# Optimization experiments

Measured on AMD Instinct MI355X. Metric: run time of the kernel, lower is better.

## Reference

```python
import jax, jax.numpy as jnp
import numpy as np

# --- fake-quant helpers (Brevitas-style simulated int4 with STE) ---

def _fq(x, scale, qmin, qmax):
    # fake quantize with straight-through estimator
    q = jnp.clip(jnp.round(x / scale), qmin, qmax) * scale
    return x + jax.lax.stop_gradient(q - x)

def quant_act_signed4(x):
    # signed 4-bit symmetric activation quant: scale = max|x| / 7
    scale = jax.lax.stop_gradient(jnp.maximum(jnp.max(jnp.abs(x)), 1e-8) / 7.0)
    return _fq(x, scale, -8, 7), scale

def quant_relu4(x):
    # QuantReLU: relu then unsigned 4-bit quant, scale = max / 15
    x = jax.nn.relu(x)
    scale = jax.lax.stop_gradient(jnp.maximum(jnp.max(x), 1e-8) / 15.0)
    return _fq(x, scale, 0, 15), scale

def quant_w4(w):
    # per-tensor symmetric 4-bit weight quant
    scale = jax.lax.stop_gradient(jnp.maximum(jnp.max(jnp.abs(w)), 1e-8) / 7.0)
    return _fq(w, scale, -8, 7), scale

def quant_bias32(b, in_scale, w_scale):
    # Int32Bias: bias quantized at scale = input_scale * weight_scale
    s = in_scale * w_scale
    return _fq(b, s, -(2.0**31), 2.0**31 - 1.0)

def conv2d(x, w, b):
    y = jax.lax.conv_general_dilated(x, w, (1, 1), 'VALID',
                                     dimension_numbers=('NCHW', 'OIHW', 'NCHW'))
    return y + b[None, :, None, None]


def setup_inputs() -> dict:
    key = jax.random.key(0)
    ks = jax.random.split(key, 9)
    f32 = jnp.float32
    return {
        'x':   jax.random.normal(ks[0], (32, 3, 224, 224), f32),
        'w1':  jax.random.normal(ks[1], (32, 3, 3, 3), f32) * 0.1,
        'b1':  jax.random.normal(ks[2], (32,), f32) * 0.05,
        'w2':  jax.random.normal(ks[3], (64, 32, 3, 3), f32) * 0.06,
        'b2':  jax.random.normal(ks[4], (64,), f32) * 0.05,
        'wf1': jax.random.normal(ks[5], (128, 64), f32) * 0.1,
        'bf1': jax.random.normal(ks[6], (128,), f32) * 0.05,
        'wf2': jax.random.normal(ks[7], (10, 128), f32) * 0.08,
        'bf2': jax.random.normal(ks[8], (10,), f32) * 0.05,
    }


def reference(x, w1, b1, w2, b2, wf1, bf1, wf2, bf2):
    # quant_inp
    xq, s_in = quant_act_signed4(x)
    # conv1 (quantized weights, Int32 bias)
    w1q, sw1 = quant_w4(w1)
    y = conv2d(xq, w1q, quant_bias32(b1, s_in, sw1))
    y, s1 = quant_relu4(y)
    # conv2
    w2q, sw2 = quant_w4(w2)
    y = conv2d(y, w2q, quant_bias32(b2, s1, sw2))
    y, s2 = quant_relu4(y)
    # adaptive avg pool to 1x1 + flatten -> [B, 64]
    y = jnp.mean(y, axis=(2, 3))
    # fc1
    wf1q, swf1 = quant_w4(wf1)
    y = y @ wf1q.T + quant_bias32(bf1, s2, swf1)
    y, s3 = quant_relu4(y)
    # fc2
    wf2q, swf2 = quant_w4(wf2)
    y = y @ wf2q.T + quant_bias32(bf2, s3, swf2)
    return jax.nn.log_softmax(y, axis=1)
```

## Files before the change

kernel.cpp:

```cpp
#include <hip/hip_runtime.h>
#include <cstdint>
#include <cstddef>

#define DI __device__ __forceinline__

typedef int v4i  __attribute__((ext_vector_type(4)));
typedef int v16i __attribute__((ext_vector_type(16)));

#if defined(__has_builtin)
#if __has_builtin(__builtin_amdgcn_sdot4)
#define HAS_SDOT4 1
#endif
#if __has_builtin(__builtin_amdgcn_alignbyte)
#define HAS_ALIGNBYTE 1
#endif
#if __has_builtin(__builtin_amdgcn_global_load_lds)
#define HAS_GLLDS 1
#endif
#if __has_builtin(__builtin_amdgcn_perm)
#define HAS_PERM 1
#endif
#endif

DI int dot4(unsigned a, unsigned b, int c) {
#ifdef HAS_SDOT4
  return __builtin_amdgcn_sdot4((int)a, (int)b, c, false);
#else
#pragma unroll
  for (int k = 0; k < 4; ++k)
    c += (int)(signed char)(a >> (8 * k)) * (int)(signed char)(b >> (8 * k));
  return c;
#endif
}

DI unsigned alignb(unsigned hi, unsigned lo, int sh) {
#ifdef HAS_ALIGNBYTE
  return __builtin_amdgcn_alignbyte(hi, lo, sh);
#else
  return sh ? ((lo >> (8 * sh)) | (hi << (32 - 8 * sh))) : lo;
#endif
}

DI unsigned bperm(unsigned hi, unsigned lo, unsigned sel) {
#ifdef HAS_PERM
  return __builtin_amdgcn_perm(hi, lo, sel);
#else
  unsigned r = 0;
#pragma unroll
  for (int i = 0; i < 4; ++i) {
    unsigned s = (sel >> (8 * i)) & 255u;
    unsigned b = (s < 4) ? (lo >> (8 * s)) : (hi >> (8 * (s - 4)));
    r |= (b & 255u) << (8 * i);
  }
  return r;
#endif
}

DI float qclamp(int a, float h) {
  return fminf(fmaxf(rintf((float)a * h), 0.f), 15.f);
}

DI unsigned pack4(float4 v, float s) {
  float f[4] = {v.x, v.y, v.z, v.w};
  unsigned w = 0;
#pragma unroll
  for (int k = 0; k < 4; ++k) {
    float q = rintf(f[k] / s);
    q = fminf(fmaxf(q, -8.f), 7.f);
    w |= ((unsigned)((int)q & 255)) << (8 * k);
  }
  return w;
}

#ifdef HAS_GLLDS
typedef __attribute__((address_space(1))) void glb_void;
typedef __attribute__((address_space(3))) void lds_void;
DI void gl_lds16(const void* g, void* l) {
  __builtin_amdgcn_global_load_lds((const glb_void*)g, (lds_void*)l, 16, 0, 0);
}
#else
DI void gl_lds16(const void* g, void* l) { *(v4i*)l = *(const v4i*)g; }
#endif

struct Scal {
  unsigned max_x, max_w1, max_w2, max_wf1, max_wf2;
  int max1, max2;
};

DI float mkscale(unsigned bits, float d) { return fmaxf(__uint_as_float(bits), 1e-8f) / d; }
DI float d_s_in(const Scal* sc) { return mkscale(sc->max_x, 7.f); }
DI float d_sw1(const Scal* sc)  { return mkscale(sc->max_w1, 7.f); }
DI float d_sw2(const Scal* sc)  { return mkscale(sc->max_w2, 7.f); }
DI float d_s1(const Scal* sc)   { return fmaxf((float)sc->max1 * (d_s_in(sc) * d_sw1(sc)), 1e-8f) / 15.f; }
DI float d_s2(const Scal* sc)   { return fmaxf((float)sc->max2 * (d_s1(sc) * d_sw2(sc)), 1e-8f) / 15.f; }

static constexpr int NX   = 32 * 3 * 224 * 224;
static constexpr int NP1  = 32 * 32 * 222 * 224;
static constexpr int C2_ROWB   = 224 * 32;
static constexpr int C2_HPLANE = 224 * 16;
static constexpr int C2V_BLK   = 1120;
static constexpr int C2V_ROWS  = 22;

DI float wave_maxf(float v) { for (int o = 32; o; o >>= 1) v = fmaxf(v, __shfl_down(v, o, 64)); return v; }
DI int   wave_maxi(int v)   { for (int o = 32; o; o >>= 1) v = max(v, __shfl_down(v, o, 64));   return v; }

DI float block_maxf(float v) {
  __shared__ float s[8];
  v = wave_maxf(v);
  int lane = threadIdx.x & 63, w = threadIdx.x >> 6;
  int nw = (int)(blockDim.x >> 6);
  if (!lane) s[w] = v;
  __syncthreads();
  if (threadIdx.x < 64) {
    float t = ((int)threadIdx.x < nw) ? s[threadIdx.x] : 0.f;
    v = wave_maxf(t);
  }
  return v;
}

DI int block_maxi(int v) {
  __shared__ int s[8];
  v = wave_maxi(v);
  int lane = threadIdx.x & 63, w = threadIdx.x >> 6;
  int nw = (int)(blockDim.x >> 6);
  if (!lane) s[w] = v;
  __syncthreads();
  if (threadIdx.x < 64) {
    int t = ((int)threadIdx.x < nw) ? s[threadIdx.x] : 0;
    v = wave_maxi(t);
  }
  return v;
}

__global__ void k_absmax_xw(const float4* __restrict__ x, int n4,
                            const float* __restrict__ w1, const float* __restrict__ w2,
                            const float* __restrict__ wf1, const float* __restrict__ wf2,
                            Scal* sc) {
  if (blockIdx.x < 1024) {
    float m = 0.f;
    for (int i = blockIdx.x * 256 + threadIdx.x; i < n4; i += 1024 * 256) {
      float4 v = x[i];
      m = fmaxf(m, fmaxf(fmaxf(fabsf(v.x), fabsf(v.y)), fmaxf(fabsf(v.z), fabsf(v.w))));
    }
    m = block_maxf(m);
    if (!threadIdx.x) atomicMax(&sc->max_x, __float_as_uint(m));
    return;
  }
  const float* p; int n; unsigned* slot;
  int wb = blockIdx.x - 1024;
  if (wb == 0)      { p = w1;  n = 864;   slot = &sc->max_w1; }
  else if (wb == 1) { p = w2;  n = 18432; slot = &sc->max_w2; }
  else if (wb == 2) { p = wf1; n = 8192;  slot = &sc->max_wf1; }
  else              { p = wf2; n = 1280;  slot = &sc->max_wf2; }
  float m = 0.f;
  for (int i = threadIdx.x; i < n; i += 256) m = fmaxf(m, fabsf(p[i]));
  m = block_maxf(m);
  if (!threadIdx.x) atomicMax(slot, __float_as_uint(m));
}


DI void kpack0(const unsigned* R, v4i& f) {
  f[0] = (int)bperm(R[1], R[0], 0x04020100u);
  f[1] = (int)bperm(R[2], R[1], 0x05040201u);
  f[2] = (int)bperm(R[3], R[2], 0x06050402u);
  f[3] = (int)bperm(R[5], R[4], 0x04020100u);
}
DI void kpack1(const unsigned* R, v4i& f) {
  f[0] = (int)bperm(R[1], R[0], 0x05040201u);
  f[1] = (int)bperm(R[2], R[1], 0x06050402u);
  f[2] = (int)bperm(0u,   R[3], 0x04020100u);
  f[3] = 0;
}

DI v4i conv1_afrag(const unsigned* lw, int oc, int lhalf) {
  unsigned R[6];
  v4i f;
  if (lhalf == 0) {
#pragma unroll
    for (int s = 0; s < 6; ++s) R[s] = lw[oc * 9 + s];
    kpack0(R, f);
  } else {
#pragma unroll
    for (int s = 0; s < 4; ++s) R[s] = lw[oc * 9 + 5 + s];
    kpack1(R, f);
  }
  return f;
}

DI v4i conv1_bfrag(const signed char* lx, int oh_l, int qb, int sh, int lhalf) {
  unsigned R[6];
  v4i f;
  if (lhalf == 0) {
#pragma unroll
    for (int s = 0; s < 6; ++s) {
      int ic = s / 3, kh = s - ic * 3;
      const signed char* base = lx + (ic * 8 + oh_l + kh) * 224 + qb;
      unsigned d0 = *(const unsigned*)base;
      unsigned d1 = *(const unsigned*)(base + 4);
      R[s] = alignb(d1, d0, sh);
    }
    kpack0(R, f);
  } else {
#pragma unroll
    for (int s = 0; s < 4; ++s) {
      int seg = 5 + s;
      int ic = seg / 3, kh = seg - ic * 3;
      const signed char* base = lx + (ic * 8 + oh_l + kh) * 224 + qb;
      unsigned d0 = *(const unsigned*)base;
      unsigned d1 = *(const unsigned*)(base + 4);
      R[s] = alignb(d1, d0, sh);
    }
    kpack1(R, f);
  }
  return f;
}

DI void conv1_stage(const float4* x, const float* w1, const float* b1,
                    int b, int oh0, int tid, float s_in, float sw1,
                    signed char* lx, unsigned* lw, int* lb) {
  for (int i = tid; i < 288; i += 448) {
    int oc = i / 9, r = i - oc * 9;
    unsigned w = 0;
#pragma unroll
    for (int k = 0; k < 3; ++k) {
      float q = rintf(w1[oc * 27 + r * 3 + k] / sw1);
      q = fminf(fmaxf(q, -8.f), 7.f);
      w |= ((unsigned)((int)q & 255)) << (8 * k);
    }
    lw[i] = w;
  }
  if (tid < 32) lb[tid] = (int)rintf(b1[tid] / (s_in * sw1));
  const float4* src = x + (size_t)b * 3 * 224 * 56;
  unsigned* dst = (unsigned*)lx;
#pragma unroll
  for (int it = 0; it < 3; ++it) {
    int i = it * 448 + tid;
    int row = i / 56, d = i - row * 56;
    int ic = row >> 3, r = row & 7;
    dst[i] = pack4(src[(ic * 224 + (oh0 + r)) * 56 + d], s_in);
  }
}

__global__ void __launch_bounds__(448) k_conv1a(
    const float4* __restrict__ x, const float* __restrict__ w1,
    const float* __restrict__ b1, const float* __restrict__ w2,
    const Scal* __restrict__ sc, unsigned* __restrict__ w2frag,
    int* __restrict__ max1) {
  int tid = threadIdx.x;
  if (blockIdx.x >= 1184) {
    int j = (blockIdx.x - 1184) * 448 + tid;
    if (j < 4608) {
      int icq = j & 7; int t = j >> 3;
      int kw = t % 3; t /= 3;
      int kh = t % 3; int oc = t / 3;
      float s = d_sw2(sc);
      unsigned w = 0;
#pragma unroll
      for (int k = 0; k < 4; ++k) {
        int ic = icq * 4 + k;
        float q = rintf(w2[(oc * 32 + ic) * 9 + kh * 3 + kw] / s);
        q = fminf(fmaxf(q, -8.f), 7.f);
        w |= ((unsigned)((int)q & 255)) << (8 * k);
      }
      int tap = kh * 3 + kw;
      int dl = (oc & 31) | ((icq >> 2) << 5);
      w2frag[(((tap * 2) + (oc >> 5)) * 64 + dl) * 4 + (icq & 3)] = w;
    }
    return;
  }

  __shared__ signed char lx[3 * 8 * 224 + 16];
  __shared__ unsigned lw[288];
  __shared__ int lb[32];
  int strip = blockIdx.x % 37;
  int b = blockIdx.x / 37;
  int oh0 = strip * 6;
  float s_in = d_s_in(sc), sw1 = d_sw1(sc);
  conv1_stage(x, w1, b1, b, oh0, tid, s_in, sw1, lx, lw, lb);
  __syncthreads();

  int lane = tid & 63, wv = tid >> 6;
  int lane31 = lane & 31, lhalf = lane >> 5;
  int p = wv * 32 + lane31;
  int qb = p & ~3, sh = p & 3;
  v4i af = conv1_afrag(lw, lane31, lhalf);
  const v4i* lbv = (const v4i*)lb;
  v16i bqv;
#pragma unroll
  for (int q = 0; q < 4; ++q) {
    v4i t = lbv[lhalf + 2 * q];
#pragma unroll
    for (int j = 0; j < 4; ++j) bqv[4 * q + j] = t[j];
  }

  int mx = 0;
#pragma unroll
  for (int oh_l = 0; oh_l < 6; ++oh_l) {
    v4i bf = conv1_bfrag(lx, oh_l, qb, sh, lhalf);
    v16i acc = __builtin_amdgcn_mfma_i32_32x32x32_i8(af, bf, bqv, 0, 0, 0);
    if (p < 222) {
#pragma unroll
      for (int r = 0; r < 16; ++r) mx = max(mx, acc[r]);
    }
  }
  mx = block_maxi(max(mx, 0));
  if (!tid) atomicMax(max1, mx);
}

__global__ void __launch_bounds__(448) k_conv1b(
    const float4* __restrict__ x, const float* __restrict__ w1,
    const float* __restrict__ b1, const Scal* __restrict__ sc,
    unsigned char* __restrict__ y1n) {
  __shared__ signed char lx[3 * 8 * 224 + 16];
  __shared__ unsigned lw[288];
  __shared__ int lb[32];
  int tid = threadIdx.x;
  int strip = blockIdx.x % 37;
  int b = blockIdx.x / 37;
  int oh0 = strip * 6;
  float s_in = d_s_in(sc), sw1 = d_sw1(sc);
  conv1_stage(x, w1, b1, b, oh0, tid, s_in, sw1, lx, lw, lb);
  __syncthreads();

  int lane = tid & 63, wv = tid >> 6;
  int lane31 = lane & 31, lhalf = lane >> 5;
  int p = wv * 32 + lane31;
  int qb = p & ~3, sh = p & 3;
  v4i af = conv1_afrag(lw, lane31, lhalf);
  const v4i* lbv = (const v4i*)lb;
  v16i bqv;
#pragma unroll
  for (int q = 0; q < 4; ++q) {
    v4i t = lbv[lhalf + 2 * q];
#pragma unroll
    for (int j = 0; j < 4; ++j) bqv[4 * q + j] = t[j];
  }

  float h1 = (s_in * sw1) / d_s1(sc);

#pragma unroll
  for (int oh_l = 0; oh_l < 6; ++oh_l) {
    v4i bf = conv1_bfrag(lx, oh_l, qb, sh, lhalf);
    v16i acc = __builtin_amdgcn_mfma_i32_32x32x32_i8(af, bf, bqv, 0, 0, 0);
    if (p < 222) {
      size_t rowb = (size_t)(b * 222 + oh0 + oh_l) * C2_ROWB;
      unsigned char* dst0 = y1n + rowb + (size_t)p * 16;
#pragma unroll
      for (int q = 0; q < 4; ++q) {
        int oc0 = 8 * q + 4 * lhalf;
        unsigned cw = 0;
#pragma unroll
        for (int j = 0; j < 4; ++j)
          cw |= ((unsigned)(int)qclamp(acc[4 * q + j], h1)) << (8 * j);
        *(unsigned*)(dst0 + (oc0 >> 4) * C2_HPLANE + (oc0 & 15)) = cw;
      }
    }
  }
}


__global__ void __launch_bounds__(256, 4) k_conv2a(
    const unsigned char* __restrict__ y1n, const unsigned* __restrict__ w2frag,
    const float* __restrict__ b2, const Scal* __restrict__ sc, int* __restrict__ max2) {
  int tid = threadIdx.x;
  int lane = tid & 63, wv = tid >> 6;
  int lane31 = lane & 31, lhalf = lane >> 5;
  int blk = (int)blockIdx.x;
  int blk2 = (blk & 7) * 140 + (blk >> 3);
  int role = blk2 * 4 + wv;
  int img = role / 140;
  int rem = role - img * 140;
  int owg = rem % 7;
  int t7 = rem / 7;
  int hh = t7 & 1;
  int vs = t7 >> 1;
  int j0 = vs * C2V_ROWS;
  int ow0 = owg * 32;

  v4i wb[9];
  const v4i* gW = (const v4i*)w2frag;
#pragma unroll
  for (int t = 0; t < 9; ++t) wb[t] = gW[(t * 2 + hh) * 64 + lane];

  float sb = d_s1(sc) * d_sw2(sc);
  int bias = (int)rintf(b2[hh * 32 + lane31] / sb);
  v16i biasv;
#pragma unroll
  for (int r = 0; r < 16; ++r) biasv[r] = bias;

  const unsigned char* base = y1n + (size_t)(img * 222 + j0) * C2_ROWB
                              + (size_t)lhalf * C2_HPLANE
                              + (size_t)(ow0 + lane31) * 16;
  v4i A[4][3];
#pragma unroll
  for (int r = 0; r < 3; ++r)
#pragma unroll
    for (int kw = 0; kw < 3; ++kw)
      A[r][kw] = *(const v4i*)(base + (size_t)r * C2_ROWB + kw * 16);

  int mx = 0;
#pragma unroll
  for (int jj = 0; jj < C2V_ROWS; ++jj) {
    if (jj < C2V_ROWS - 1) {
      const unsigned char* rp = base + (size_t)(jj + 3) * C2_ROWB;
#pragma unroll
      for (int kw = 0; kw < 3; ++kw)
        A[(jj + 3) & 3][kw] = *(const v4i*)(rp + kw * 16);
    }
    v16i acc = __builtin_amdgcn_mfma_i32_32x32x32_i8(A[jj & 3][0], wb[0], biasv, 0, 0, 0);
#pragma unroll
    for (int kh = 0; kh < 3; ++kh)
#pragma unroll
      for (int kw = 0; kw < 3; ++kw) {
        if (kh == 0 && kw == 0) continue;
        acc = __builtin_amdgcn_mfma_i32_32x32x32_i8(A[(jj + kh) & 3][kw], wb[kh * 3 + kw], acc, 0, 0, 0);
      }

    if (owg != 6) {
#pragma unroll
      for (int r = 0; r < 16; ++r) mx = max(mx, acc[r]);
    } else {
#pragma unroll
      for (int r = 0; r < 16; ++r) {
        int m = (r & 3) + 8 * (r >> 2) + 4 * lhalf;
        if (ow0 + m < 220) mx = max(mx, acc[r]);
      }
    }
  }
  mx = block_maxi(max(mx, 0));
  if (!tid) atomicMax(max2, mx);
}

__global__ void __launch_bounds__(256, 4) k_conv2b(
    const unsigned char* __restrict__ y1n, const unsigned* __restrict__ w2frag,
    const float* __restrict__ b2, const Scal* __restrict__ sc,
    int* __restrict__ pooled_i) {
  int tid = threadIdx.x;
  int lane = tid & 63, wv = tid >> 6;
  int lane31 = lane & 31, lhalf = lane >> 5;
  int blk = (int)blockIdx.x;
  int blk2 = (blk & 7) * 140 + (blk >> 3);
  int role = blk2 * 4 + wv;
  int img = role / 140;
  int rem = role - img * 140;
  int owg = rem % 7;
  int t7 = rem / 7;
  int hh = t7 & 1;
  int vs = t7 >> 1;
  int j0 = vs * C2V_ROWS;
  int ow0 = owg * 32;

  v4i wb[9];
  const v4i* gW = (const v4i*)w2frag;
#pragma unroll
  for (int t = 0; t < 9; ++t) wb[t] = gW[(t * 2 + hh) * 64 + lane];

  float sb = d_s1(sc) * d_sw2(sc);
  int bias = (int)rintf(b2[hh * 32 + lane31] / sb);
  float h1 = sb * (1.0f / d_s2(sc));
  v16i biasv;
#pragma unroll
  for (int r = 0; r < 16; ++r) biasv[r] = bias;

  const unsigned char* base = y1n + (size_t)(img * 222 + j0) * C2_ROWB
                              + (size_t)lhalf * C2_HPLANE
                              + (size_t)(ow0 + lane31) * 16;
  v4i A[4][3];
#pragma unroll
  for (int r = 0; r < 3; ++r)
#pragma unroll
    for (int kw = 0; kw < 3; ++kw)
      A[r][kw] = *(const v4i*)(base + (size_t)r * C2_ROWB + kw * 16);

  float psum = 0.f;
#pragma unroll
  for (int jj = 0; jj < C2V_ROWS; ++jj) {
    if (jj < C2V_ROWS - 1) {
      const unsigned char* rp = base + (size_t)(jj + 3) * C2_ROWB;
#pragma unroll
      for (int kw = 0; kw < 3; ++kw)
        A[(jj + 3) & 3][kw] = *(const v4i*)(rp + kw * 16);
    }
    v16i acc = __builtin_amdgcn_mfma_i32_32x32x32_i8(A[jj & 3][0], wb[0], biasv, 0, 0, 0);
#pragma unroll
    for (int kh = 0; kh < 3; ++kh)
#pragma unroll
      for (int kw = 0; kw < 3; ++kw) {
        if (kh == 0 && kw == 0) continue;
        acc = __builtin_amdgcn_mfma_i32_32x32x32_i8(A[(jj + kh) & 3][kw], wb[kh * 3 + kw], acc, 0, 0, 0);
      }

    if (owg != 6) {
#pragma unroll
      for (int r = 0; r < 16; ++r) psum += qclamp(acc[r], h1);
    } else {
#pragma unroll
      for (int r = 0; r < 16; ++r) {
        int m = (r & 3) + 8 * (r >> 2) + 4 * lhalf;
        if (ow0 + m < 220) psum += qclamp(acc[r], h1);
      }
    }
  }
  int s = (int)psum;
  s += __shfl_down(s, 32, 64);
  if (lhalf == 0) atomicAdd(&pooled_i[img * 64 + hh * 32 + lane31], s);
}

__global__ void __launch_bounds__(1024) k_fc(
    const int* __restrict__ pooled_i, const float* __restrict__ wf1,
    const float* __restrict__ bf1, const float* __restrict__ wf2,
    const float* __restrict__ bf2, const Scal* __restrict__ sc,
    float* __restrict__ out) {
  __shared__ float pl[2048];
  __shared__ __align__(16) float wq1[128 * 68];
  __shared__ __align__(16) float y3[32 * 132];
  __shared__ float zz[320];
  __shared__ float s3sh;
  __shared__ float red16[16];
  int tid = threadIdx.x;
  float swf1 = mkscale(sc->max_wf1, 7.f), swf2 = mkscale(sc->max_wf2, 7.f);
  float s2 = d_s2(sc);
  for (int i = tid; i < 2048; i += 1024) pl[i] = (float)pooled_i[i] * s2 / 48400.0f;
  for (int i = tid; i < 8192; i += 1024) {
    float q = rintf(wf1[i] / swf1);
    q = fminf(fmaxf(q, -8.f), 7.f);
    wq1[(i >> 6) * 68 + (i & 63)] = q * swf1;
  }
  __syncthreads();
  float sb1 = s2 * swf1;
  float lmax = 0.f;
#pragma unroll
  for (int o = tid; o < 4096; o += 1024) {
    int b = o >> 7, j = o & 127;
    float acc = rintf(bf1[j] / sb1) * sb1;
    const float4* wr4 = (const float4*)&wq1[j * 68];
    const float4* xr4 = (const float4*)&pl[b * 64];
#pragma unroll
    for (int k4 = 0; k4 < 16; ++k4) {
      float4 w4 = wr4[k4], x4 = xr4[k4];
      acc += x4.x * w4.x + x4.y * w4.y + x4.z * w4.z + x4.w * w4.w;
    }
    float r = fmaxf(acc, 0.f);
    y3[b * 132 + j] = r;
    lmax = fmaxf(lmax, r);
  }
  lmax = wave_maxf(lmax);
  {
    int lane = tid & 63, w = tid >> 6;
    if (!lane) red16[w] = lmax;
  }
  __syncthreads();
  if (tid < 64) {
    float t = (tid < 16) ? red16[tid] : 0.f;
    t = wave_maxf(t);
    if (!tid) s3sh = fmaxf(t, 1e-8f) / 15.f;
  }
  __syncthreads();
  float s3 = s3sh;
  float sb2 = s3 * swf2;
  if (tid < 320) {
    int o = tid;
    int b = o / 10, j = o - b * 10;
    float acc = rintf(bf2[j] / sb2) * sb2;
    const float4* yy4 = (const float4*)&y3[b * 132];
    const float4* wr4 = (const float4*)&wf2[j * 128];
#pragma unroll 8
    for (int k4 = 0; k4 < 32; ++k4) {
      float4 y4 = yy4[k4];
      float4 w4 = wr4[k4];
      float yv[4] = {y4.x, y4.y, y4.z, y4.w};
      float wv4[4] = {w4.x, w4.y, w4.z, w4.w};
#pragma unroll
      for (int e = 0; e < 4; ++e) {
        float q = rintf(yv[e] / s3);
        q = fminf(fmaxf(q, 0.f), 15.f);
        float wv = rintf(wv4[e] / swf2);
        wv = fminf(fmaxf(wv, -8.f), 7.f);
        acc += (q * s3) * (wv * swf2);
      }
    }
    zz[o] = acc;
  }
  __syncthreads();
  if (tid < 32) {
    const float* z = &zz[tid * 10];
    float mm = z[0];
    for (int k = 1; k < 10; ++k) mm = fmaxf(mm, z[k]);
    float ssum = 0.f;
    for (int k = 0; k < 10; ++k) ssum += expf(z[k] - mm);
    float l = mm + logf(ssum);
    for (int k = 0; k < 10; ++k) out[tid * 10 + k] = z[k] - l;
  }
}

extern "C" void kernel_launch(void* const* d_in, const int* in_sizes, int n_in,
                              void* d_out, int out_size, void* d_ws, size_t ws_size,
                              hipStream_t stream) {
  const float* x   = (const float*)d_in[0];
  const float* w1  = (const float*)d_in[1];
  const float* b1  = (const float*)d_in[2];
  const float* w2  = (const float*)d_in[3];
  const float* b2  = (const float*)d_in[4];
  const float* wf1 = (const float*)d_in[5];
  const float* bf1 = (const float*)d_in[6];
  const float* wf2 = (const float*)d_in[7];
  const float* bf2 = (const float*)d_in[8];
  float* out = (float*)d_out;

  char* ws = (char*)d_ws;
  Scal* sc = (Scal*)ws;
  int* pooled_i = (int*)(ws + 1024);
  size_t off = 1024 + 8192;
  unsigned* w2frag = (unsigned*)(ws + off);     off += 4608 * 4;
  off = (off + 255) & ~(size_t)255;
  unsigned char* y1n = (unsigned char*)(ws + off); off += (size_t)NP1 + 256;
  (void)ws_size; (void)in_sizes; (void)n_in; (void)out_size;

  hipMemsetAsync(ws, 0, 1024 + 8192, stream);
  k_absmax_xw<<<1028, 256, 0, stream>>>((const float4*)x, NX / 4, w1, w2, wf1, wf2, sc);
  k_conv1a<<<1184 + 11, 448, 0, stream>>>((const float4*)x, w1, b1, w2, sc, w2frag, &sc->max1);
  k_conv1b<<<1184, 448, 0, stream>>>((const float4*)x, w1, b1, sc, y1n);
  k_conv2a<<<C2V_BLK, 256, 0, stream>>>(y1n, w2frag, b2, sc, &sc->max2);
  k_conv2b<<<C2V_BLK, 256, 0, stream>>>(y1n, w2frag, b2, sc, pooled_i);
  k_fc<<<1, 1024, 0, stream>>>(pooled_i, wf1, bf1, wf2, bf2, sc, out);
}
```

Measured before the change: 235.4 us.

## Halve rows per conv2 wave and split MFMA chain into two accumulators

Each conv2 wave now handles 11 output rows instead of 22, which doubles the grid (C2V_BLK 1120 to 2240, role mapping 140 to 280 per image) to expose more waves. The nine-MFMA dependent chain is also split into two independent accumulator chains that are summed afterwards, so consecutive MFMAs can overlap. The cost is more per-wave setup (weight fragment loads, bias computation, the three-row initial halo load, atomics) relative to useful work, plus an extra 16-register accumulator and vector adds.

Result: slower. 244.4 us (+3.8%).

```diff
diff --git a/kernel.cpp b/kernel.cpp
--- a/kernel.cpp
+++ b/kernel.cpp
@@ -98,8 +98,8 @@
 static constexpr int NP1  = 32 * 32 * 222 * 224;
 static constexpr int C2_ROWB   = 224 * 32;
 static constexpr int C2_HPLANE = 224 * 16;
-static constexpr int C2V_BLK   = 1120;
-static constexpr int C2V_ROWS  = 22;
+static constexpr int C2V_BLK   = 2240;
+static constexpr int C2V_ROWS  = 11;
 
 DI float wave_maxf(float v) { for (int o = 32; o; o >>= 1) v = fmaxf(v, __shfl_down(v, o, 64)); return v; }
 DI int   wave_maxi(int v)   { for (int o = 32; o; o >>= 1) v = max(v, __shfl_down(v, o, 64));   return v; }
@@ -366,10 +366,10 @@
   int lane = tid & 63, wv = tid >> 6;
   int lane31 = lane & 31, lhalf = lane >> 5;
   int blk = (int)blockIdx.x;
-  int blk2 = (blk & 7) * 140 + (blk >> 3);
+  int blk2 = (blk & 7) * 280 + (blk >> 3);
   int role = blk2 * 4 + wv;
-  int img = role / 140;
-  int rem = role - img * 140;
+  int img = role / 280;
+  int rem = role - img * 280;
   int owg = rem % 7;
   int t7 = rem / 7;
   int hh = t7 & 1;
@@ -384,9 +384,9 @@
 
   float sb = d_s1(sc) * d_sw2(sc);
   int bias = (int)rintf(b2[hh * 32 + lane31] / sb);
-  v16i biasv;
-#pragma unroll
-  for (int r = 0; r < 16; ++r) biasv[r] = bias;
+  v16i biasv, zerov;
+#pragma unroll
+  for (int r = 0; r < 16; ++r) { biasv[r] = bias; zerov[r] = 0; }
 
   const unsigned char* base = y1n + (size_t)(img * 222 + j0) * C2_ROWB
                               + (size_t)lhalf * C2_HPLANE
@@ -407,23 +407,24 @@
       for (int kw = 0; kw < 3; ++kw)
         A[(jj + 3) & 3][kw] = *(const v4i*)(rp + kw * 16);
     }
-    v16i acc = __builtin_amdgcn_mfma_i32_32x32x32_i8(A[jj & 3][0], wb[0], biasv, 0, 0, 0);
-#pragma unroll
-    for (int kh = 0; kh < 3; ++kh)
-#pragma unroll
-      for (int kw = 0; kw < 3; ++kw) {
-        if (kh == 0 && kw == 0) continue;
-        acc = __builtin_amdgcn_mfma_i32_32x32x32_i8(A[(jj + kh) & 3][kw], wb[kh * 3 + kw], acc, 0, 0, 0);
-      }
+    v16i a0 = __builtin_amdgcn_mfma_i32_32x32x32_i8(A[jj & 3][0], wb[0], biasv, 0, 0, 0);
+    a0 = __builtin_amdgcn_mfma_i32_32x32x32_i8(A[jj & 3][1], wb[1], a0, 0, 0, 0);
+    a0 = __builtin_amdgcn_mfma_i32_32x32x32_i8(A[jj & 3][2], wb[2], a0, 0, 0, 0);
+    a0 = __builtin_amdgcn_mfma_i32_32x32x32_i8(A[(jj + 1) & 3][0], wb[3], a0, 0, 0, 0);
+    a0 = __builtin_amdgcn_mfma_i32_32x32x32_i8(A[(jj + 1) & 3][1], wb[4], a0, 0, 0, 0);
+    v16i a1 = __builtin_amdgcn_mfma_i32_32x32x32_i8(A[(jj + 1) & 3][2], wb[5], zerov, 0, 0, 0);
+    a1 = __builtin_amdgcn_mfma_i32_32x32x32_i8(A[(jj + 2) & 3][0], wb[6], a1, 0, 0, 0);
+    a1 = __builtin_amdgcn_mfma_i32_32x32x32_i8(A[(jj + 2) & 3][1], wb[7], a1, 0, 0, 0);
+    a1 = __builtin_amdgcn_mfma_i32_32x32x32_i8(A[(jj + 2) & 3][2], wb[8], a1, 0, 0, 0);
 
     if (owg != 6) {
 #pragma unroll
-      for (int r = 0; r < 16; ++r) mx = max(mx, acc[r]);
+      for (int r = 0; r < 16; ++r) mx = max(mx, a0[r] + a1[r]);
     } else {
 #pragma unroll
       for (int r = 0; r < 16; ++r) {
         int m = (r & 3) + 8 * (r >> 2) + 4 * lhalf;
-        if (ow0 + m < 220) mx = max(mx, acc[r]);
+        if (ow0 + m < 220) mx = max(mx, a0[r] + a1[r]);
       }
     }
   }
@@ -439,10 +440,10 @@
   int lane = tid & 63, wv = tid >> 6;
   int lane31 = lane & 31, lhalf = lane >> 5;
   int blk = (int)blockIdx.x;
-  int blk2 = (blk & 7) * 140 + (blk >> 3);
+  int blk2 = (blk & 7) * 280 + (blk >> 3);
   int role = blk2 * 4 + wv;
-  int img = role / 140;
-  int rem = role - img * 140;
+  int img = role / 280;
+  int rem = role - img * 280;
   int owg = rem % 7;
   int t7 = rem / 7;
   int hh = t7 & 1;
@@ -458,9 +459,9 @@
   float sb = d_s1(sc) * d_sw2(sc);
   int bias = (int)rintf(b2[hh * 32 + lane31] / sb);
   float h1 = sb * (1.0f / d_s2(sc));
-  v16i biasv;
-#pragma unroll
-  for (int r = 0; r < 16; ++r) biasv[r] = bias;
+  v16i biasv, zerov;
+#pragma unroll
+  for (int r = 0; r < 16; ++r) { biasv[r] = bias; zerov[r] = 0; }
 
   const unsigned char* base = y1n + (size_t)(img * 222 + j0) * C2_ROWB
                               + (size_t)lhalf * C2_HPLANE
@@ -481,23 +482,24 @@
       for (int kw = 0; kw < 3; ++kw)
         A[(jj + 3) & 3][kw] = *(const v4i*)(rp + kw * 16);
     }
-    v16i acc = __builtin_amdgcn_mfma_i32_32x32x32_i8(A[jj & 3][0], wb[0], biasv, 0, 0, 0);
-#pragma unroll
-    for (int kh = 0; kh < 3; ++kh)
-#pragma unroll
-      for (int kw = 0; kw < 3; ++kw) {
-        if (kh == 0 && kw == 0) continue;
-        acc = __builtin_amdgcn_mfma_i32_32x32x32_i8(A[(jj + kh) & 3][kw], wb[kh * 3 + kw], acc, 0, 0, 0);
-      }
+    v16i a0 = __builtin_amdgcn_mfma_i32_32x32x32_i8(A[jj & 3][0], wb[0], biasv, 0, 0, 0);
+    a0 = __builtin_amdgcn_mfma_i32_32x32x32_i8(A[jj & 3][1], wb[1], a0, 0, 0, 0);
+    a0 = __builtin_amdgcn_mfma_i32_32x32x32_i8(A[jj & 3][2], wb[2], a0, 0, 0, 0);
+    a0 = __builtin_amdgcn_mfma_i32_32x32x32_i8(A[(jj + 1) & 3][0], wb[3], a0, 0, 0, 0);
+    a0 = __builtin_amdgcn_mfma_i32_32x32x32_i8(A[(jj + 1) & 3][1], wb[4], a0, 0, 0, 0);
+    v16i a1 = __builtin_amdgcn_mfma_i32_32x32x32_i8(A[(jj + 1) & 3][2], wb[5], zerov, 0, 0, 0);
+    a1 = __builtin_amdgcn_mfma_i32_32x32x32_i8(A[(jj + 2) & 3][0], wb[6], a1, 0, 0, 0);
+    a1 = __builtin_amdgcn_mfma_i32_32x32x32_i8(A[(jj + 2) & 3][1], wb[7], a1, 0, 0, 0);
+    a1 = __builtin_amdgcn_mfma_i32_32x32x32_i8(A[(jj + 2) & 3][2], wb[8], a1, 0, 0, 0);
 
     if (owg != 6) {
 #pragma unroll
-      for (int r = 0; r < 16; ++r) psum += qclamp(acc[r], h1);
+      for (int r = 0; r < 16; ++r) psum += qclamp(a0[r] + a1[r], h1);
     } else {
 #pragma unroll
       for (int r = 0; r < 16; ++r) {
         int m = (r & 3) + 8 * (r >> 2) + 4 * lhalf;
-        if (ow0 + m < 220) psum += qclamp(acc[r], h1);
+        if (ow0 + m < 220) psum += qclamp(a0[r] + a1[r], h1);
       }
     }
   }
```
